# Kernel tuning notes

Hardware: AMD Instinct MI355X
Metric: run time of the kernel (lower is better)

Reference implementation:

```python
import jax, jax.numpy as jnp
import numpy as np

GAMMA = 0.5
MOMENTUM = 0.9
REPEAT_THR = 1.0
LOSS_WEIGHT = 1.0
BINS = jnp.asarray(np.arange(0.2, 1.0, 0.05), dtype=jnp.float32)  # 16 bin left edges
NUM_BIN = 16


def setup_inputs() -> dict:
    key = jax.random.key(0)
    k1, k2 = jax.random.split(key)
    shape = (64, 512, 512)
    outputs = jax.random.normal(k1, shape, dtype=jnp.float32)
    targets = jax.random.uniform(k2, shape, dtype=jnp.float32)  # in [0,1), spans all bins
    counts = jnp.ones((NUM_BIN,), dtype=jnp.float32) * 10000.0  # buffer init
    return {"outputs": outputs, "targets": targets, "counts": counts}


def reference(outputs, targets, counts):
    # Single digitize pass replaces the per-bin mask loop.
    # searchsorted(side='right') - 1 => index i s.t. bins[i] <= t < bins[i+1];
    # last bin is open-ended (t >= bins[-1] -> i = NUM_BIN-1); t < bins[0] -> -1.
    flat_t = targets.reshape(-1)
    idx = jnp.searchsorted(BINS, flat_t, side="right") - 1
    valid = idx >= 0
    safe_idx = jnp.where(valid, idx, 0)

    # histogram of targets over bins (single scatter-add pass)
    bin_counts = jnp.zeros((NUM_BIN,), dtype=jnp.float32).at[safe_idx].add(
        valid.astype(jnp.float32))

    # EMA buffer update (mirrors self.counts in-place update)
    new_counts = MOMENTUM * counts + (1.0 - MOMENTUM) * bin_counts
    freq = new_counts / new_counts.sum()
    wi = (REPEAT_THR / freq) ** GAMMA  # [NUM_BIN]

    # gather per-element weight; elements below bins[0] keep weight 1
    weights = jnp.where(valid, wi[safe_idx], 1.0).reshape(targets.shape)

    l1 = jnp.abs(outputs - targets)
    loss = jnp.sum(l1 * weights) / jnp.sum(weights)
    return loss * LOSS_WEIGHT
```

## Files before the change

kernel.cpp:

```cpp
#include <hip/hip_runtime.h>
#include <math.h>


#define NBIN 16
#define NSLOT 17
#define THREADS 256
#define NBLOCKS 1024


__global__ __launch_bounds__(THREADS, 4)
void bll_hist(const float* __restrict__ outputs, const float* __restrict__ targets,
              float* __restrict__ ws, int n4) {
    __shared__ float S_lds[THREADS * NSLOT];
    __shared__ float N_lds[THREADS * NSLOT];
    const int tid = threadIdx.x;
    const int base = tid * NSLOT;

    #pragma unroll
    for (int s = 0; s < NSLOT; ++s) {
        S_lds[base + s] = 0.0f;
        N_lds[base + s] = 0.0f;
    }

    const float bins[NBIN] = {0.20f, 0.25f, 0.30f, 0.35f, 0.40f, 0.45f, 0.50f, 0.55f,
                              0.60f, 0.65f, 0.70f, 0.75f, 0.80f, 0.85f, 0.90f, 0.95f};

    const float4* __restrict__ t4p = (const float4*)targets;
    const float4* __restrict__ o4p = (const float4*)outputs;
    const int stride = gridDim.x * THREADS;

    for (int i = blockIdx.x * THREADS + tid; i < n4; i += stride) {
        const float4 t = t4p[i];
        const float4 o = o4p[i];
        const float tv[4] = {t.x, t.y, t.z, t.w};
        const float ov[4] = {o.x, o.y, o.z, o.w};
        #pragma unroll
        for (int c = 0; c < 4; ++c) {
            const float tc = tv[c];
            int k = 0;
            #pragma unroll
            for (int b = 0; b < NBIN; ++b) k += (tc >= bins[b]) ? 1 : 0;
            const float l1 = fabsf(ov[c] - tc);
            const int sl = base + k;
            S_lds[sl] += l1;
            N_lds[sl] += 1.0f;
        }
    }
    __syncthreads();

    for (int off = THREADS / 2; off > 0; off >>= 1) {
        if (tid < off) {
            #pragma unroll
            for (int s = 0; s < NSLOT; ++s) {
                S_lds[tid * NSLOT + s] += S_lds[(tid + off) * NSLOT + s];
                N_lds[tid * NSLOT + s] += N_lds[(tid + off) * NSLOT + s];
            }
        }
        __syncthreads();
    }

    if (tid < NSLOT) {
        unsafeAtomicAdd(&ws[tid], S_lds[tid]);
    } else if (tid < 2 * NSLOT) {
        unsafeAtomicAdd(&ws[tid], N_lds[tid - NSLOT]);
    }
}

__global__ void bll_final(const float* __restrict__ ws, const float* __restrict__ counts,
                          float* __restrict__ out) {
    if (threadIdx.x == 0 && blockIdx.x == 0) {
        const float S_inv = ws[0];
        const float N_inv = ws[NSLOT];
        float newc[NBIN];
        float total = 0.0f;
        #pragma unroll
        for (int b = 0; b < NBIN; ++b) {
            newc[b] = 0.9f * counts[b] + 0.1f * ws[NSLOT + 1 + b];
            total += newc[b];
        }
        float num = S_inv;
        float den = N_inv;
        #pragma unroll
        for (int b = 0; b < NBIN; ++b) {
            const float wi = sqrtf(total / newc[b]);
            num += wi * ws[1 + b];
            den += wi * ws[NSLOT + 1 + b];
        }
        out[0] = num / den;
    }
}

extern "C" void kernel_launch(void* const* d_in, const int* in_sizes, int n_in,
                              void* d_out, int out_size, void* d_ws, size_t ws_size,
                              hipStream_t stream) {
    const float* outputs = (const float*)d_in[0];
    const float* targets = (const float*)d_in[1];
    const float* counts  = (const float*)d_in[2];
    float* out = (float*)d_out;
    float* ws  = (float*)d_ws;

    const int n  = in_sizes[0];
    const int n4 = n >> 2;

    hipMemsetAsync(ws, 0, 2 * NSLOT * sizeof(float), stream);
    bll_hist<<<NBLOCKS, THREADS, 0, stream>>>(outputs, targets, ws, n4);
    bll_final<<<1, 64, 0, stream>>>(ws, counts, out);
}
```

Before: 177.5 us.

## Replace per-thread LDS histogram with register cumulative bins and wave ballot counts

Drops the per-thread LDS histogram slots (a 34 KB shared array with a read-modify-write per element and a log-step tree reduction). Each thread now keeps cumulative per-threshold sums in registers and counts with wave ballot/popcount. Blocks reduce with wave shuffles before doing atomics to padded workspace slots, and the final kernel differences the cumulative values to recover per-bin sums. Grid size is doubled and atomic targets are spread across cache lines. In exchange it does 16 compare/select/ballot operations per element, which may make the kernel more ALU-bound, and float differencing adds rounding risk.

```diff
diff --git a/kernel.cpp b/kernel.cpp
--- a/kernel.cpp
+++ b/kernel.cpp
@@ -3,33 +3,27 @@
 
 
 #define NBIN 16
-#define NSLOT 17
 #define THREADS 256
-#define NBLOCKS 1024
+#define NBLOCKS 2048
+#define WS_STRIDE 64
 
-
-__global__ __launch_bounds__(THREADS, 4)
-void bll_hist(const float* __restrict__ outputs, const float* __restrict__ targets,
+__global__ __launch_bounds__(THREADS)
+void bll_pass(const float* __restrict__ outputs, const float* __restrict__ targets,
               float* __restrict__ ws, int n4) {
-    __shared__ float S_lds[THREADS * NSLOT];
-    __shared__ float N_lds[THREADS * NSLOT];
-    const int tid = threadIdx.x;
-    const int base = tid * NSLOT;
-
-    #pragma unroll
-    for (int s = 0; s < NSLOT; ++s) {
-        S_lds[base + s] = 0.0f;
-        N_lds[base + s] = 0.0f;
-    }
-
     const float bins[NBIN] = {0.20f, 0.25f, 0.30f, 0.35f, 0.40f, 0.45f, 0.50f, 0.55f,
                               0.60f, 0.65f, 0.70f, 0.75f, 0.80f, 0.85f, 0.90f, 0.95f};
+
+    float cs[NBIN];
+    int   cn[NBIN];
+    float ts = 0.0f;
+    #pragma unroll
+    for (int b = 0; b < NBIN; ++b) { cs[b] = 0.0f; cn[b] = 0; }
 
     const float4* __restrict__ t4p = (const float4*)targets;
     const float4* __restrict__ o4p = (const float4*)outputs;
     const int stride = gridDim.x * THREADS;
 
-    for (int i = blockIdx.x * THREADS + tid; i < n4; i += stride) {
+    for (int i = blockIdx.x * THREADS + threadIdx.x; i < n4; i += stride) {
         const float4 t = t4p[i];
         const float4 o = o4p[i];
         const float tv[4] = {t.x, t.y, t.z, t.w};
@@ -37,45 +31,67 @@
         #pragma unroll
         for (int c = 0; c < 4; ++c) {
             const float tc = tv[c];
-            int k = 0;
+            const float l1 = fabsf(ov[c] - tc);
+            ts += l1;
             #pragma unroll
-            for (int b = 0; b < NBIN; ++b) k += (tc >= bins[b]) ? 1 : 0;
-            const float l1 = fabsf(ov[c] - tc);
-            const int sl = base + k;
-            S_lds[sl] += l1;
-            N_lds[sl] += 1.0f;
+            for (int b = 0; b < NBIN; ++b) {
+                const bool p = (tc >= bins[b]);
+                cs[b] += p ? l1 : 0.0f;
+                cn[b] += (int)__popcll(__ballot(p));
+            }
         }
     }
+
+    #pragma unroll
+    for (int b = 0; b < NBIN; ++b) {
+        #pragma unroll
+        for (int off = 32; off; off >>= 1) cs[b] += __shfl_xor(cs[b], off);
+    }
+    #pragma unroll
+    for (int off = 32; off; off >>= 1) ts += __shfl_xor(ts, off);
+
+    __shared__ float red[4][33];
+    const int lane = threadIdx.x & 63;
+    const int wv   = threadIdx.x >> 6;
+    if (lane == 0) {
+        #pragma unroll
+        for (int b = 0; b < NBIN; ++b) {
+            red[wv][b]        = cs[b];
+            red[wv][NBIN + b] = (float)cn[b];
+        }
+        red[wv][32] = ts;
+    }
     __syncthreads();
-
-    for (int off = THREADS / 2; off > 0; off >>= 1) {
-        if (tid < off) {
-            #pragma unroll
-            for (int s = 0; s < NSLOT; ++s) {
-                S_lds[tid * NSLOT + s] += S_lds[(tid + off) * NSLOT + s];
-                N_lds[tid * NSLOT + s] += N_lds[(tid + off) * NSLOT + s];
-            }
-        }
-        __syncthreads();
-    }
-
-    if (tid < NSLOT) {
-        unsafeAtomicAdd(&ws[tid], S_lds[tid]);
-    } else if (tid < 2 * NSLOT) {
-        unsafeAtomicAdd(&ws[tid], N_lds[tid - NSLOT]);
+    if (threadIdx.x < 33) {
+        const float v = red[0][threadIdx.x] + red[1][threadIdx.x] +
+                        red[2][threadIdx.x] + red[3][threadIdx.x];
+        unsafeAtomicAdd(&ws[threadIdx.x * WS_STRIDE], v);
     }
 }
 
 __global__ void bll_final(const float* __restrict__ ws, const float* __restrict__ counts,
-                          float* __restrict__ out) {
+                          float* __restrict__ out, float totN) {
     if (threadIdx.x == 0 && blockIdx.x == 0) {
-        const float S_inv = ws[0];
-        const float N_inv = ws[NSLOT];
-        float newc[NBIN];
+        float cumS[NBIN + 1], cumN[NBIN + 1];
+        #pragma unroll
+        for (int b = 0; b < NBIN; ++b) {
+            cumS[b] = ws[b * WS_STRIDE];
+            cumN[b] = ws[(NBIN + b) * WS_STRIDE];
+        }
+        cumS[NBIN] = 0.0f;
+        cumN[NBIN] = 0.0f;
+        const float totS = ws[32 * WS_STRIDE];
+
+        const float S_inv = totS - cumS[0];
+        const float N_inv = totN - cumN[0];
+
+        float Nb[NBIN], Sb[NBIN], newc[NBIN];
         float total = 0.0f;
         #pragma unroll
         for (int b = 0; b < NBIN; ++b) {
-            newc[b] = 0.9f * counts[b] + 0.1f * ws[NSLOT + 1 + b];
+            Sb[b] = cumS[b] - cumS[b + 1];
+            Nb[b] = cumN[b] - cumN[b + 1];
+            newc[b] = 0.9f * counts[b] + 0.1f * Nb[b];
             total += newc[b];
         }
         float num = S_inv;
@@ -83,8 +99,8 @@
         #pragma unroll
         for (int b = 0; b < NBIN; ++b) {
             const float wi = sqrtf(total / newc[b]);
-            num += wi * ws[1 + b];
-            den += wi * ws[NSLOT + 1 + b];
+            num += wi * Sb[b];
+            den += wi * Nb[b];
         }
         out[0] = num / den;
     }
@@ -102,7 +118,7 @@
     const int n  = in_sizes[0];
     const int n4 = n >> 2;
 
-    hipMemsetAsync(ws, 0, 2 * NSLOT * sizeof(float), stream);
-    bll_hist<<<NBLOCKS, THREADS, 0, stream>>>(outputs, targets, ws, n4);
-    bll_final<<<1, 64, 0, stream>>>(ws, counts, out);
+    hipMemsetAsync(ws, 0, 33 * WS_STRIDE * sizeof(float), stream);
+    bll_pass<<<NBLOCKS, THREADS, 0, stream>>>(outputs, targets, ws, n4);
+    bll_final<<<1, 64, 0, stream>>>(ws, counts, out, (float)n);
 }
```

New measurement: 166.1 us. 6.4% less time.
